# Kernel optimization log

Hardware: AMD Instinct MI355X
Metric: run time of the kernel (lower is better)

Reference implementation:

```python
import jax, jax.numpy as jnp
import numpy as np

T, IN, E, H, L = 8192, 40, 256, 512, 2


def setup_inputs() -> dict:
    key = jax.random.key(0)
    ks = jax.random.split(key, 12)
    s = lambda k, shape, scale: jax.random.normal(k, shape, dtype=jnp.float32) * scale
    return {
        "in_states": jax.random.normal(ks[0], (T, IN), dtype=jnp.float32),
        "W_in": s(ks[1], (E, IN), 0.1),
        "b_in": jnp.zeros((E,), jnp.float32),          # nn.Linear bias init to 0
        "W_ih0": s(ks[2], (4 * H, E), 0.04),
        "W_hh0": s(ks[3], (4 * H, H), 0.04),
        "b_ih0": s(ks[4], (4 * H,), 0.04),
        "b_hh0": s(ks[5], (4 * H,), 0.04),
        "W_ih1": s(ks[6], (4 * H, H), 0.04),
        "W_hh1": s(ks[7], (4 * H, H), 0.04),
        "b_ih1": s(ks[8], (4 * H,), 0.04),
        "b_hh1": s(ks[9], (4 * H,), 0.04),
        "W_out": s(ks[10], (1, H), 0.04),
        "b_out": jnp.zeros((1,), jnp.float32),         # nn.Linear bias init to 0
    }


def lstm_layer(x, W_ih, W_hh, b_ih, b_hh):
    """PyTorch-convention LSTM layer over a [T, in] sequence, batch=1.
    Gate order: i, f, g, o. Returns ([T, H] hidden seq, h_T, c_T)."""
    Hd = W_hh.shape[1]
    # Precompute the input contribution for all timesteps at once: [T, 4H]
    xg = x @ W_ih.T + (b_ih + b_hh)

    def cell(carry, xg_t):
        h, c = carry
        g = xg_t + h @ W_hh.T
        i, f, gg, o = jnp.split(g, 4)
        i = jax.nn.sigmoid(i)
        f = jax.nn.sigmoid(f)
        gg = jnp.tanh(gg)
        o = jax.nn.sigmoid(o)
        c = f * c + i * gg
        h = o * jnp.tanh(c)
        return (h, c), h

    h0 = jnp.zeros((Hd,), x.dtype)
    (hT, cT), hs = jax.lax.scan(cell, (h0, h0), xg)
    return hs, hT, cT


def reference(in_states, W_in, b_in, W_ih0, W_hh0, b_ih0, b_hh0,
              W_ih1, W_hh1, b_ih1, b_hh1, W_out, b_out):
    # Input projection for every timestep (the per-step nn.Linear, batched): [T, E]
    x = in_states @ W_in.T + b_in
    # Two stacked LSTM layers
    h1, hT0, cT0 = lstm_layer(x, W_ih0, W_hh0, b_ih0, b_hh0)
    h2, hT1, cT1 = lstm_layer(h1, W_ih1, W_hh1, b_ih1, b_hh1)
    # Output projection per timestep -> [T, 1, 1] like the torch `outputs` buffer
    outputs = (h2 @ W_out.T + b_out)[:, None, :]
    # Final hidden state tuple, shaped [num_layers, batch=1, H]
    h_final = jnp.stack([hT0, hT1])[:, None, :]
    c_final = jnp.stack([cT0, cT1])[:, None, :]
    return outputs, (h_final, c_final)
```

## Files before the change

kernel.cpp:

```cpp
#include <hip/hip_runtime.h>

#define T_LEN 8192
#define NIN   40
#define E_DIM 256
#define HID   512
#define G4H   2048

__device__ __forceinline__ float4 ld4_sc(const float* p) {
  float4 v;
  asm volatile("global_load_dwordx4 %0, %1, off sc0 sc1" : "=v"(v) : "v"(p));
  return v;
}
__device__ __forceinline__ unsigned ld_flag(const unsigned* p) {
  unsigned v;
  asm volatile("global_load_dword %0, %1, off sc0 sc1\n\ts_waitcnt vmcnt(0)"
               : "=v"(v) : "v"(p) : "memory");
  return v;
}
__device__ __forceinline__ void st_sc(float* p, float v) {
  asm volatile("global_store_dword %0, %1, off sc0 sc1" :: "v"(p), "v"(v) : "memory");
}
__device__ __forceinline__ void st_flag(unsigned* p, unsigned v) {
  asm volatile("global_store_dword %0, %1, off sc0 sc1" :: "v"(p), "v"(v) : "memory");
}
#define VM_FENCE() do { asm volatile("s_waitcnt vmcnt(0)" ::: "memory"); \
                        __builtin_amdgcn_sched_barrier(0); } while (0)

__device__ __forceinline__ float sigm(float x) {
  x = fminf(20.f, fmaxf(-20.f, x));
  float e = __builtin_amdgcn_exp2f(-1.442695040888963f * x);
  return __builtin_amdgcn_rcpf(1.f + e);
}
__device__ __forceinline__ float tanh_f(float x) {
  x = fminf(10.f, fmaxf(-10.f, x));
  float e = __builtin_amdgcn_exp2f(-2.885390081777927f * x);
  return (1.f - e) * __builtin_amdgcn_rcpf(1.f + e);
}
__device__ __forceinline__ float sel4(int k, float a0, float a1, float a2, float a3) {
  float r = a0;
  r = (k == 1) ? a1 : r;
  r = (k == 2) ? a2 : r;
  r = (k == 3) ? a3 : r;
  return r;
}

__global__ __launch_bounds__(64) void prep_kernel(
    const float* __restrict__ W_in, const float* __restrict__ b_in,
    const float* __restrict__ W_ih0, const float* __restrict__ b_ih0,
    const float* __restrict__ b_hh0,
    float* __restrict__ W_comb, float* __restrict__ bias_comb)
{
  const int r = blockIdx.x;
  const int lane = threadIdx.x;
  float bp = 0.f;
  for (int e = lane; e < E_DIM; e += 64) bp += W_ih0[(size_t)r * E_DIM + e] * b_in[e];
  float acc = 0.f;
  if (lane < NIN) {
    for (int e = 0; e < E_DIM; ++e)
      acc += W_ih0[(size_t)r * E_DIM + e] * W_in[(size_t)e * NIN + lane];
  }
#pragma unroll
  for (int m = 1; m < 64; m <<= 1) bp += __shfl_xor(bp, m, 64);
  if (lane < NIN) W_comb[(size_t)r * NIN + lane] = acc;
  if (lane == 0) bias_comb[r] = bp + b_ih0[r] + b_hh0[r];
}

__global__ __launch_bounds__(1024, 4) void scan_kernel(
    const float* __restrict__ in_states,
    const float* __restrict__ W_hh0,
    const float* __restrict__ W_ih1,
    const float* __restrict__ W_hh1,
    const float* __restrict__ b_ih1,
    const float* __restrict__ b_hh1,
    const float* __restrict__ W_comb,
    const float* __restrict__ bias_comb,
    float* __restrict__ h1buf, float* __restrict__ h2buf,
    unsigned* __restrict__ flags0, unsigned* __restrict__ flags1,
    float* __restrict__ d_out)
{
  const int tid  = threadIdx.x;
  const int wid  = tid >> 6;
  const int lane = tid & 63;
  const int bid  = blockIdx.x;

  __shared__ float lds_wcomb[128 * (NIN + 1)];
  __shared__ float lds_in[NIN];
  __shared__ float lds_indot[128];

  if (bid < 16) {
    const int u0 = bid * 32;
    const int uA = u0 + wid * 2;
    const int G  = (lane & 2) | ((lane >> 2) & 1);
    const int ulocal4 = (wid * 2 + (lane & 1)) * 4;

    for (int i = tid; i < 128 * NIN; i += 1024) {
      int lr = i / NIN, k = i - lr * NIN;
      int R = (lr & 3) * HID + u0 + (lr >> 2);
      lds_wcomb[lr * (NIN + 1) + k] = W_comb[(size_t)R * NIN + k];
    }
    float w[8][8];
#pragma unroll
    for (int q = 0; q < 8; ++q) {
      int R = (q & 3) * HID + uA + (q >> 2);
      const float4* p = (const float4*)(W_hh0 + (size_t)R * HID + lane * 8);
      float4 a = p[0], b = p[1];
      w[q][0]=a.x; w[q][1]=a.y; w[q][2]=a.z; w[q][3]=a.w;
      w[q][4]=b.x; w[q][5]=b.y; w[q][6]=b.z; w[q][7]=b.w;
    }
    float my_bias = 0.f;
    if (tid >= 128 && tid < 256) {
      int r = tid - 128;
      my_bias = bias_comb[(size_t)((r & 3) * HID + u0 + (r >> 2))];
    }
    float inreg = 0.f;
    if (tid >= 64 && tid < 64 + NIN) inreg = in_states[NIN + (tid - 64)];
    if (tid < NIN) lds_in[tid] = in_states[tid];
    __syncthreads();
    if (tid >= 128 && tid < 256) {
      int r = tid - 128;
      float s = my_bias;
#pragma unroll
      for (int k = 0; k < NIN; ++k) s += lds_wcomb[r * (NIN + 1) + k] * lds_in[k];
      lds_indot[r] = s;
    }

    float c_reg = 0.f;
    for (int t = 0; t < T_LEN; ++t) {
      if (wid == 0 && t > 0 && lane < 16) {
        const unsigned* fp = flags0 + (size_t)(t - 1) * 16 + lane;
        while (ld_flag(fp) == 0u) {}
      }
      __syncthreads();
      if (tid >= 64 && tid < 64 + NIN) {
        lds_in[tid - 64] = inreg;
        int t2 = (t + 2 < T_LEN) ? (t + 2) : (T_LEN - 1);
        inreg = in_states[(size_t)t2 * NIN + (tid - 64)];
      }
      float hv[8];
      if (t > 0) {
        const float* hp = h1buf + (size_t)(t - 1) * HID + lane * 8;
        float4 A = ld4_sc(hp);
        float4 B = ld4_sc(hp + 4);
        VM_FENCE();
        hv[0]=A.x; hv[1]=A.y; hv[2]=A.z; hv[3]=A.w;
        hv[4]=B.x; hv[5]=B.y; hv[6]=B.z; hv[7]=B.w;
      } else {
#pragma unroll
        for (int j = 0; j < 8; ++j) hv[j] = 0.f;
      }
      float acc[8] = {0,0,0,0,0,0,0,0};
#pragma unroll
      for (int cc = 0; cc < 8; ++cc) {
#pragma unroll
        for (int q = 0; q < 8; ++q) acc[q] = fmaf(w[q][cc], hv[cc], acc[q]);
      }
      float a4[4];
#pragma unroll
      for (int g = 0; g < 4; ++g) {
        float send = (lane & 1) ? acc[g] : acc[g + 4];
        float recv = __shfl_xor(send, 1, 64);
        a4[g] = ((lane & 1) ? acc[g + 4] : acc[g]) + recv;
      }
      float b2[2];
#pragma unroll
      for (int j = 0; j < 2; ++j) {
        float send = (lane & 2) ? a4[j] : a4[j + 2];
        float recv = __shfl_xor(send, 2, 64);
        b2[j] = ((lane & 2) ? a4[j + 2] : a4[j]) + recv;
      }
      float c1;
      {
        float send = (lane & 4) ? b2[0] : b2[1];
        float recv = __shfl_xor(send, 4, 64);
        c1 = ((lane & 4) ? b2[1] : b2[0]) + recv;
      }
      c1 += __shfl_xor(c1, 8, 64);
      c1 += __shfl_xor(c1, 16, 64);
      c1 += __shfl_xor(c1, 32, 64);
      float pre = c1 + lds_indot[ulocal4 + G];
      float s2 = __shfl_xor(pre, 2, 64);
      float s4 = __shfl_xor(pre, 4, 64);
      float s6 = __shfl_xor(pre, 6, 64);
      float prei = sel4(G,     pre, s4, s2, s6);
      float pref = sel4(G ^ 1, pre, s4, s2, s6);
      float preg = sel4(G ^ 2, pre, s4, s2, s6);
      float preo = sel4(G ^ 3, pre, s4, s2, s6);
      float gi = sigm(prei), gf = sigm(pref), gg = tanh_f(preg), go = sigm(preo);
      c_reg = gf * c_reg + gi * gg;
      float hnew = go * tanh_f(c_reg);
      if (lane < 2) {
        st_sc(h1buf + (size_t)t * HID + uA + lane, hnew);
        if (t == T_LEN - 1) {
          d_out[T_LEN + uA + lane] = hnew;
          d_out[T_LEN + 2 * HID + uA + lane] = c_reg;
        }
      }
      VM_FENCE();
      __syncthreads();
      if (tid == 0) st_flag(flags0 + (size_t)t * 16 + bid, 1u);
      if (tid >= 128 && tid < 256 && t + 1 < T_LEN) {
        int r = tid - 128;
        float s = my_bias;
#pragma unroll
        for (int k = 0; k < NIN; ++k) s += lds_wcomb[r * (NIN + 1) + k] * lds_in[k];
        lds_indot[r] = s;
      }
    }
  } else {
    const int wg = bid - 16;
    const int u0 = wg * 16;
    const int u  = u0 + wid;
    const int G  = ((lane & 1) << 1) | ((lane >> 1) & 1);
    float w[4][16];
    {
      const float* Wsrc = (lane < 32) ? W_ih1 : W_hh1;
      int colbase = (lane & 31) * 16;
#pragma unroll
      for (int g = 0; g < 4; ++g) {
        int R = g * HID + u;
        const float4* p = (const float4*)(Wsrc + (size_t)R * HID + colbase);
        float4 x0 = p[0], x1 = p[1], x2 = p[2], x3 = p[3];
        w[g][0]=x0.x;  w[g][1]=x0.y;  w[g][2]=x0.z;  w[g][3]=x0.w;
        w[g][4]=x1.x;  w[g][5]=x1.y;  w[g][6]=x1.z;  w[g][7]=x1.w;
        w[g][8]=x2.x;  w[g][9]=x2.y;  w[g][10]=x2.z; w[g][11]=x2.w;
        w[g][12]=x3.x; w[g][13]=x3.y; w[g][14]=x3.z; w[g][15]=x3.w;
      }
    }
    const float bias_lane = b_ih1[G * HID + u] + b_hh1[G * HID + u];
    float c_reg = 0.f;
    for (int t = 0; t < T_LEN; ++t) {
      if (wid == 0) {
        const unsigned* fp = nullptr;
        if (lane < 16) fp = flags0 + (size_t)t * 16 + lane;
        else if (lane < 48 && t > 0) fp = flags1 + (size_t)(t - 1) * 32 + (lane - 16);
        if (fp) { while (ld_flag(fp) == 0u) {} }
      }
      __syncthreads();
      float hv[16];
      {
        int col = (lane & 31) * 16;
        int tp = (t > 0) ? (t - 1) : 0;
        const float* hp = (lane < 32) ? (h1buf + (size_t)t * HID + col)
                                      : (h2buf + (size_t)tp * HID + col);
        bool hvalid = (lane < 32) || (t > 0);
        float4 A = ld4_sc(hp);
        float4 B = ld4_sc(hp + 4);
        float4 C = ld4_sc(hp + 8);
        float4 D = ld4_sc(hp + 12);
        VM_FENCE();
        float tmp[16];
        tmp[0]=A.x; tmp[1]=A.y; tmp[2]=A.z; tmp[3]=A.w;
        tmp[4]=B.x; tmp[5]=B.y; tmp[6]=B.z; tmp[7]=B.w;
        tmp[8]=C.x; tmp[9]=C.y; tmp[10]=C.z; tmp[11]=C.w;
        tmp[12]=D.x; tmp[13]=D.y; tmp[14]=D.z; tmp[15]=D.w;
#pragma unroll
        for (int j = 0; j < 16; ++j) hv[j] = hvalid ? tmp[j] : 0.f;
      }
      float acc[4] = {0,0,0,0};
#pragma unroll
      for (int cc = 0; cc < 16; ++cc) {
#pragma unroll
        for (int g = 0; g < 4; ++g) acc[g] = fmaf(w[g][cc], hv[cc], acc[g]);
      }
      float b2[2];
#pragma unroll
      for (int j = 0; j < 2; ++j) {
        float send = (lane & 1) ? acc[j] : acc[j + 2];
        float recv = __shfl_xor(send, 1, 64);
        b2[j] = ((lane & 1) ? acc[j + 2] : acc[j]) + recv;
      }
      float c1;
      {
        float send = (lane & 2) ? b2[0] : b2[1];
        float recv = __shfl_xor(send, 2, 64);
        c1 = ((lane & 2) ? b2[1] : b2[0]) + recv;
      }
      c1 += __shfl_xor(c1, 4, 64);
      c1 += __shfl_xor(c1, 8, 64);
      c1 += __shfl_xor(c1, 16, 64);
      c1 += __shfl_xor(c1, 32, 64);
      float pre = c1 + bias_lane;
      float s1 = __shfl_xor(pre, 1, 64);
      float s2 = __shfl_xor(pre, 2, 64);
      float s3 = __shfl_xor(pre, 3, 64);
      float prei = sel4(G,     pre, s2, s1, s3);
      float pref = sel4(G ^ 1, pre, s2, s1, s3);
      float preg = sel4(G ^ 2, pre, s2, s1, s3);
      float preo = sel4(G ^ 3, pre, s2, s1, s3);
      float gi = sigm(prei), gf = sigm(pref), gg = tanh_f(preg), go = sigm(preo);
      c_reg = gf * c_reg + gi * gg;
      float hnew = go * tanh_f(c_reg);
      if (lane == 0) {
        st_sc(h2buf + (size_t)t * HID + u, hnew);
        if (t == T_LEN - 1) {
          d_out[T_LEN + HID + u] = hnew;
          d_out[T_LEN + 3 * HID + u] = c_reg;
        }
      }
      VM_FENCE();
      __syncthreads();
      if (tid == 0) st_flag(flags1 + (size_t)t * 32 + wg, 1u);
    }
  }
}

__global__ __launch_bounds__(256) void out_kernel(
    const float* __restrict__ h2buf, const float* __restrict__ W_out,
    const float* __restrict__ b_out, float* __restrict__ d_out)
{
  int t = blockIdx.x * 4 + (threadIdx.x >> 6);
  int lane = threadIdx.x & 63;
  const float4* hp = (const float4*)(h2buf + (size_t)t * HID + lane * 8);
  const float4* wp = (const float4*)(W_out + lane * 8);
  float4 a = hp[0], b = hp[1], wa = wp[0], wb = wp[1];
  float s = a.x*wa.x + a.y*wa.y + a.z*wa.z + a.w*wa.w
          + b.x*wb.x + b.y*wb.y + b.z*wb.z + b.w*wb.w;
#pragma unroll
  for (int m = 1; m < 64; m <<= 1) s += __shfl_xor(s, m, 64);
  if (lane == 0) d_out[t] = s + b_out[0];
}

extern "C" void kernel_launch(void* const* d_in, const int* in_sizes, int n_in,
                              void* d_out, int out_size, void* d_ws, size_t ws_size,
                              hipStream_t stream) {
  const float* in_states = (const float*)d_in[0];
  const float* W_in  = (const float*)d_in[1];
  const float* b_in  = (const float*)d_in[2];
  const float* W_ih0 = (const float*)d_in[3];
  const float* W_hh0 = (const float*)d_in[4];
  const float* b_ih0 = (const float*)d_in[5];
  const float* b_hh0 = (const float*)d_in[6];
  const float* W_ih1 = (const float*)d_in[7];
  const float* W_hh1 = (const float*)d_in[8];
  const float* b_ih1 = (const float*)d_in[9];
  const float* b_hh1 = (const float*)d_in[10];
  const float* W_out = (const float*)d_in[11];
  const float* b_out = (const float*)d_in[12];

  float* ws = (float*)d_ws;
  size_t o = 0;
  float* W_comb = ws + o;    o += (size_t)G4H * NIN;
  float* bias_comb = ws + o; o += G4H;
  float* h1buf = ws + o;     o += (size_t)T_LEN * HID;
  float* h2buf = ws + o;     o += (size_t)T_LEN * HID;
  unsigned* flags0 = (unsigned*)(ws + o); o += (size_t)T_LEN * 16;
  unsigned* flags1 = (unsigned*)(ws + o); o += (size_t)T_LEN * 32;

  hipMemsetAsync(flags0, 0, (size_t)T_LEN * 48 * sizeof(unsigned), stream);

  prep_kernel<<<G4H, 64, 0, stream>>>(W_in, b_in, W_ih0, b_ih0, b_hh0,
                                      W_comb, bias_comb);
  scan_kernel<<<48, 1024, 0, stream>>>(in_states, W_hh0, W_ih1, W_hh1,
                                       b_ih1, b_hh1, W_comb, bias_comb,
                                       h1buf, h2buf, flags0, flags1,
                                       (float*)d_out);
  out_kernel<<<2048, 256, 0, stream>>>(h2buf, W_out, b_out, (float*)d_out);
}
```

Before: 25.22 ms.

## Replace flag barriers with sequence-tagged data polling across single-wave blocks

Restructures the persistent LSTM scan so each single-wave block owns two hidden units, with 512 blocks instead of 48 large blocks. Each hidden value is stored next to a sequence tag, so consumers poll the data itself rather than separate flag arrays behind __syncthreads, removing a round trip and the block-level barriers. The input projection is folded into the per-step FMA, layer 2 uses an 8-slot ring buffer, and the output projection becomes per-step atomics, removing the separate output kernel. The risks are heavier polling traffic from 512 spinning waves, possible deadlock if not all blocks are co-resident, and atomic ordering making the output sum order nondeterministic.

```diff
diff --git a/kernel.cpp b/kernel.cpp
--- a/kernel.cpp
+++ b/kernel.cpp
@@ -5,23 +5,17 @@
 #define E_DIM 256
 #define HID   512
 #define G4H   2048
+#define RD    8
 
 __device__ __forceinline__ float4 ld4_sc(const float* p) {
   float4 v;
   asm volatile("global_load_dwordx4 %0, %1, off sc0 sc1" : "=v"(v) : "v"(p));
   return v;
 }
-__device__ __forceinline__ unsigned ld_flag(const unsigned* p) {
-  unsigned v;
-  asm volatile("global_load_dword %0, %1, off sc0 sc1\n\ts_waitcnt vmcnt(0)"
-               : "=v"(v) : "v"(p) : "memory");
-  return v;
-}
-__device__ __forceinline__ void st_sc(float* p, float v) {
-  asm volatile("global_store_dword %0, %1, off sc0 sc1" :: "v"(p), "v"(v) : "memory");
-}
-__device__ __forceinline__ void st_flag(unsigned* p, unsigned v) {
-  asm volatile("global_store_dword %0, %1, off sc0 sc1" :: "v"(p), "v"(v) : "memory");
+__device__ __forceinline__ void st2_sc(float* p, float h, unsigned seq) {
+  union { float2 f; uint2 u; } pv;
+  pv.u.x = __float_as_uint(h); pv.u.y = seq;
+  asm volatile("global_store_dwordx2 %0, %1, off sc0 sc1" :: "v"(p), "v"(pv.f) : "memory");
 }
 #define VM_FENCE() do { asm volatile("s_waitcnt vmcnt(0)" ::: "memory"); \
                         __builtin_amdgcn_sched_barrier(0); } while (0)
@@ -65,7 +59,7 @@
   if (lane == 0) bias_comb[r] = bp + b_ih0[r] + b_hh0[r];
 }
 
-__global__ __launch_bounds__(1024, 4) void scan_kernel(
+__global__ __launch_bounds__(64, 1) void scan_kernel(
     const float* __restrict__ in_states,
     const float* __restrict__ W_hh0,
     const float* __restrict__ W_ih1,
@@ -74,30 +68,18 @@
     const float* __restrict__ b_hh1,
     const float* __restrict__ W_comb,
     const float* __restrict__ bias_comb,
-    float* __restrict__ h1buf, float* __restrict__ h2buf,
-    unsigned* __restrict__ flags0, unsigned* __restrict__ flags1,
+    const float* __restrict__ W_out,
+    const float* __restrict__ b_out,
+    float* __restrict__ h1pair,
+    float* __restrict__ h2ring,
     float* __restrict__ d_out)
 {
-  const int tid  = threadIdx.x;
-  const int wid  = tid >> 6;
-  const int lane = tid & 63;
+  const int lane = threadIdx.x;
   const int bid  = blockIdx.x;
-
-  __shared__ float lds_wcomb[128 * (NIN + 1)];
-  __shared__ float lds_in[NIN];
-  __shared__ float lds_indot[128];
-
-  if (bid < 16) {
-    const int u0 = bid * 32;
-    const int uA = u0 + wid * 2;
-    const int G  = (lane & 2) | ((lane >> 2) & 1);
-    const int ulocal4 = (wid * 2 + (lane & 1)) * 4;
-
-    for (int i = tid; i < 128 * NIN; i += 1024) {
-      int lr = i / NIN, k = i - lr * NIN;
-      int R = (lr & 3) * HID + u0 + (lr >> 2);
-      lds_wcomb[lr * (NIN + 1) + k] = W_comb[(size_t)R * NIN + k];
-    }
+  const int G    = (lane & 2) | ((lane >> 2) & 1);
+
+  if (bid < 256) {
+    const int uA = bid * 2;
     float w[8][8];
 #pragma unroll
     for (int q = 0; q < 8; ++q) {
@@ -107,48 +89,42 @@
       w[q][0]=a.x; w[q][1]=a.y; w[q][2]=a.z; w[q][3]=a.w;
       w[q][4]=b.x; w[q][5]=b.y; w[q][6]=b.z; w[q][7]=b.w;
     }
-    float my_bias = 0.f;
-    if (tid >= 128 && tid < 256) {
-      int r = tid - 128;
-      my_bias = bias_comb[(size_t)((r & 3) * HID + u0 + (r >> 2))];
-    }
-    float inreg = 0.f;
-    if (tid >= 64 && tid < 64 + NIN) inreg = in_states[NIN + (tid - 64)];
-    if (tid < NIN) lds_in[tid] = in_states[tid];
-    __syncthreads();
-    if (tid >= 128 && tid < 256) {
-      int r = tid - 128;
-      float s = my_bias;
-#pragma unroll
-      for (int k = 0; k < NIN; ++k) s += lds_wcomb[r * (NIN + 1) + k] * lds_in[k];
-      lds_indot[r] = s;
-    }
-
+    float w2[8];
+#pragma unroll
+    for (int q = 0; q < 8; ++q) {
+      int R = (q & 3) * HID + uA + (q >> 2);
+      w2[q] = (lane < NIN) ? W_comb[(size_t)R * NIN + lane] : 0.f;
+    }
+    const float bias_lane = bias_comb[G * HID + uA + (lane & 1)];
+    float in_cur = (lane < NIN) ? in_states[lane] : 0.f;
     float c_reg = 0.f;
+
     for (int t = 0; t < T_LEN; ++t) {
-      if (wid == 0 && t > 0 && lane < 16) {
-        const unsigned* fp = flags0 + (size_t)(t - 1) * 16 + lane;
-        while (ld_flag(fp) == 0u) {}
-      }
-      __syncthreads();
-      if (tid >= 64 && tid < 64 + NIN) {
-        lds_in[tid - 64] = inreg;
-        int t2 = (t + 2 < T_LEN) ? (t + 2) : (T_LEN - 1);
-        inreg = in_states[(size_t)t2 * NIN + (tid - 64)];
-      }
+      float in_nxt = (lane < NIN && t + 1 < T_LEN)
+                   ? in_states[(size_t)(t + 1) * NIN + lane] : 0.f;
       float hv[8];
       if (t > 0) {
-        const float* hp = h1buf + (size_t)(t - 1) * HID + lane * 8;
-        float4 A = ld4_sc(hp);
-        float4 B = ld4_sc(hp + 4);
-        VM_FENCE();
-        hv[0]=A.x; hv[1]=A.y; hv[2]=A.z; hv[3]=A.w;
-        hv[4]=B.x; hv[5]=B.y; hv[6]=B.z; hv[7]=B.w;
+        const float* hp = h1pair + ((size_t)(t - 1) << 10) + lane * 16;
+        const unsigned e = (unsigned)t;
+        float4 A, B, C, D; int ok;
+        do {
+          A = ld4_sc(hp); B = ld4_sc(hp + 4); C = ld4_sc(hp + 8); D = ld4_sc(hp + 12);
+          VM_FENCE();
+          unsigned bad = (__float_as_uint(A.y) ^ e) | (__float_as_uint(A.w) ^ e)
+                       | (__float_as_uint(B.y) ^ e) | (__float_as_uint(B.w) ^ e)
+                       | (__float_as_uint(C.y) ^ e) | (__float_as_uint(C.w) ^ e)
+                       | (__float_as_uint(D.y) ^ e) | (__float_as_uint(D.w) ^ e);
+          ok = (bad == 0u);
+        } while (!__all(ok));
+        hv[0]=A.x; hv[1]=A.z; hv[2]=B.x; hv[3]=B.z;
+        hv[4]=C.x; hv[5]=C.z; hv[6]=D.x; hv[7]=D.z;
       } else {
 #pragma unroll
         for (int j = 0; j < 8; ++j) hv[j] = 0.f;
       }
-      float acc[8] = {0,0,0,0,0,0,0,0};
+      float acc[8];
+#pragma unroll
+      for (int q = 0; q < 8; ++q) acc[q] = w2[q] * in_cur;
 #pragma unroll
       for (int cc = 0; cc < 8; ++cc) {
 #pragma unroll
@@ -177,7 +153,7 @@
       c1 += __shfl_xor(c1, 8, 64);
       c1 += __shfl_xor(c1, 16, 64);
       c1 += __shfl_xor(c1, 32, 64);
-      float pre = c1 + lds_indot[ulocal4 + G];
+      float pre = c1 + bias_lane;
       float s2 = __shfl_xor(pre, 2, 64);
       float s4 = __shfl_xor(pre, 4, 64);
       float s6 = __shfl_xor(pre, 6, 64);
@@ -189,135 +165,121 @@
       c_reg = gf * c_reg + gi * gg;
       float hnew = go * tanh_f(c_reg);
       if (lane < 2) {
-        st_sc(h1buf + (size_t)t * HID + uA + lane, hnew);
+        st2_sc(h1pair + ((size_t)t << 10) + (uA + lane) * 2, hnew, (unsigned)(t + 1));
         if (t == T_LEN - 1) {
           d_out[T_LEN + uA + lane] = hnew;
           d_out[T_LEN + 2 * HID + uA + lane] = c_reg;
         }
       }
-      VM_FENCE();
-      __syncthreads();
-      if (tid == 0) st_flag(flags0 + (size_t)t * 16 + bid, 1u);
-      if (tid >= 128 && tid < 256 && t + 1 < T_LEN) {
-        int r = tid - 128;
-        float s = my_bias;
-#pragma unroll
-        for (int k = 0; k < NIN; ++k) s += lds_wcomb[r * (NIN + 1) + k] * lds_in[k];
-        lds_indot[r] = s;
-      }
+      in_cur = in_nxt;
     }
   } else {
-    const int wg = bid - 16;
-    const int u0 = wg * 16;
-    const int u  = u0 + wid;
-    const int G  = ((lane & 1) << 1) | ((lane >> 1) & 1);
-    float w[4][16];
-    {
-      const float* Wsrc = (lane < 32) ? W_ih1 : W_hh1;
-      int colbase = (lane & 31) * 16;
+    const int uB = (bid - 256) * 2;
+    const float* Wsrc = (lane < 32) ? W_ih1 : W_hh1;
+    const int c0 = (lane & 31) * 16;
+    float w[8][16];
+#pragma unroll
+    for (int q = 0; q < 8; ++q) {
+      int R = (q & 3) * HID + uB + (q >> 2);
+      const float4* p = (const float4*)(Wsrc + (size_t)R * HID + c0);
+      float4 x0 = p[0], x1 = p[1], x2 = p[2], x3 = p[3];
+      w[q][0]=x0.x;  w[q][1]=x0.y;  w[q][2]=x0.z;  w[q][3]=x0.w;
+      w[q][4]=x1.x;  w[q][5]=x1.y;  w[q][6]=x1.z;  w[q][7]=x1.w;
+      w[q][8]=x2.x;  w[q][9]=x2.y;  w[q][10]=x2.z; w[q][11]=x2.w;
+      w[q][12]=x3.x; w[q][13]=x3.y; w[q][14]=x3.z; w[q][15]=x3.w;
+    }
+    const int brow = G * HID + uB + (lane & 1);
+    const float bias_lane = b_ih1[brow] + b_hh1[brow];
+    const float wout_lane = W_out[uB + (lane & 1)];
+    const float b_out0 = b_out[0];
+    float c_reg = 0.f;
+
+    for (int t = 0; t < T_LEN; ++t) {
+      const bool is_h1 = (lane < 32);
+      const bool hvalid = is_h1 || (t > 0);
+      const int rslot = (t > 0) ? ((t - 1) % RD) : 0;
+      const float* hp = is_h1
+          ? (h1pair + ((size_t)t << 10) + lane * 32)
+          : (h2ring + (size_t)rslot * 1024 + (lane - 32) * 32);
+      const unsigned e = is_h1 ? (unsigned)(t + 1) : (unsigned)t;
+      float4 P0, P1, P2, P3, P4, P5, P6, P7; int ok;
+      do {
+        P0 = ld4_sc(hp);      P1 = ld4_sc(hp + 4);
+        P2 = ld4_sc(hp + 8);  P3 = ld4_sc(hp + 12);
+        P4 = ld4_sc(hp + 16); P5 = ld4_sc(hp + 20);
+        P6 = ld4_sc(hp + 24); P7 = ld4_sc(hp + 28);
+        VM_FENCE();
+        unsigned bad = (__float_as_uint(P0.y) ^ e) | (__float_as_uint(P0.w) ^ e)
+                     | (__float_as_uint(P1.y) ^ e) | (__float_as_uint(P1.w) ^ e)
+                     | (__float_as_uint(P2.y) ^ e) | (__float_as_uint(P2.w) ^ e)
+                     | (__float_as_uint(P3.y) ^ e) | (__float_as_uint(P3.w) ^ e)
+                     | (__float_as_uint(P4.y) ^ e) | (__float_as_uint(P4.w) ^ e)
+                     | (__float_as_uint(P5.y) ^ e) | (__float_as_uint(P5.w) ^ e)
+                     | (__float_as_uint(P6.y) ^ e) | (__float_as_uint(P6.w) ^ e)
+                     | (__float_as_uint(P7.y) ^ e) | (__float_as_uint(P7.w) ^ e);
+        ok = (bad == 0u) || !hvalid;
+      } while (!__all(ok));
+      float hv[16];
+      hv[0]=P0.x;  hv[1]=P0.z;  hv[2]=P1.x;  hv[3]=P1.z;
+      hv[4]=P2.x;  hv[5]=P2.z;  hv[6]=P3.x;  hv[7]=P3.z;
+      hv[8]=P4.x;  hv[9]=P4.z;  hv[10]=P5.x; hv[11]=P5.z;
+      hv[12]=P6.x; hv[13]=P6.z; hv[14]=P7.x; hv[15]=P7.z;
+      if (!hvalid) {
+#pragma unroll
+        for (int j = 0; j < 16; ++j) hv[j] = 0.f;
+      }
+      float acc[8] = {0,0,0,0,0,0,0,0};
+#pragma unroll
+      for (int cc = 0; cc < 16; ++cc) {
+#pragma unroll
+        for (int q = 0; q < 8; ++q) acc[q] = fmaf(w[q][cc], hv[cc], acc[q]);
+      }
+      float a4[4];
 #pragma unroll
       for (int g = 0; g < 4; ++g) {
-        int R = g * HID + u;
-        const float4* p = (const float4*)(Wsrc + (size_t)R * HID + colbase);
-        float4 x0 = p[0], x1 = p[1], x2 = p[2], x3 = p[3];
-        w[g][0]=x0.x;  w[g][1]=x0.y;  w[g][2]=x0.z;  w[g][3]=x0.w;
-        w[g][4]=x1.x;  w[g][5]=x1.y;  w[g][6]=x1.z;  w[g][7]=x1.w;
-        w[g][8]=x2.x;  w[g][9]=x2.y;  w[g][10]=x2.z; w[g][11]=x2.w;
-        w[g][12]=x3.x; w[g][13]=x3.y; w[g][14]=x3.z; w[g][15]=x3.w;
-      }
-    }
-    const float bias_lane = b_ih1[G * HID + u] + b_hh1[G * HID + u];
-    float c_reg = 0.f;
-    for (int t = 0; t < T_LEN; ++t) {
-      if (wid == 0) {
-        const unsigned* fp = nullptr;
-        if (lane < 16) fp = flags0 + (size_t)t * 16 + lane;
-        else if (lane < 48 && t > 0) fp = flags1 + (size_t)(t - 1) * 32 + (lane - 16);
-        if (fp) { while (ld_flag(fp) == 0u) {} }
-      }
-      __syncthreads();
-      float hv[16];
-      {
-        int col = (lane & 31) * 16;
-        int tp = (t > 0) ? (t - 1) : 0;
-        const float* hp = (lane < 32) ? (h1buf + (size_t)t * HID + col)
-                                      : (h2buf + (size_t)tp * HID + col);
-        bool hvalid = (lane < 32) || (t > 0);
-        float4 A = ld4_sc(hp);
-        float4 B = ld4_sc(hp + 4);
-        float4 C = ld4_sc(hp + 8);
-        float4 D = ld4_sc(hp + 12);
-        VM_FENCE();
-        float tmp[16];
-        tmp[0]=A.x; tmp[1]=A.y; tmp[2]=A.z; tmp[3]=A.w;
-        tmp[4]=B.x; tmp[5]=B.y; tmp[6]=B.z; tmp[7]=B.w;
-        tmp[8]=C.x; tmp[9]=C.y; tmp[10]=C.z; tmp[11]=C.w;
-        tmp[12]=D.x; tmp[13]=D.y; tmp[14]=D.z; tmp[15]=D.w;
-#pragma unroll
-        for (int j = 0; j < 16; ++j) hv[j] = hvalid ? tmp[j] : 0.f;
-      }
-      float acc[4] = {0,0,0,0};
-#pragma unroll
-      for (int cc = 0; cc < 16; ++cc) {
-#pragma unroll
-        for (int g = 0; g < 4; ++g) acc[g] = fmaf(w[g][cc], hv[cc], acc[g]);
-      }
-      float b2[2];
+        float send = (lane & 1) ? acc[g] : acc[g + 4];
+        float recv = __shfl_xor(send, 1, 64);
+        a4[g] = ((lane & 1) ? acc[g + 4] : acc[g]) + recv;
+      }
+      float b2v[2];
 #pragma unroll
       for (int j = 0; j < 2; ++j) {
-        float send = (lane & 1) ? acc[j] : acc[j + 2];
-        float recv = __shfl_xor(send, 1, 64);
-        b2[j] = ((lane & 1) ? acc[j + 2] : acc[j]) + recv;
+        float send = (lane & 2) ? a4[j] : a4[j + 2];
+        float recv = __shfl_xor(send, 2, 64);
+        b2v[j] = ((lane & 2) ? a4[j + 2] : a4[j]) + recv;
       }
       float c1;
       {
-        float send = (lane & 2) ? b2[0] : b2[1];
-        float recv = __shfl_xor(send, 2, 64);
-        c1 = ((lane & 2) ? b2[1] : b2[0]) + recv;
-      }
-      c1 += __shfl_xor(c1, 4, 64);
+        float send = (lane & 4) ? b2v[0] : b2v[1];
+        float recv = __shfl_xor(send, 4, 64);
+        c1 = ((lane & 4) ? b2v[1] : b2v[0]) + recv;
+      }
       c1 += __shfl_xor(c1, 8, 64);
       c1 += __shfl_xor(c1, 16, 64);
       c1 += __shfl_xor(c1, 32, 64);
       float pre = c1 + bias_lane;
-      float s1 = __shfl_xor(pre, 1, 64);
       float s2 = __shfl_xor(pre, 2, 64);
-      float s3 = __shfl_xor(pre, 3, 64);
-      float prei = sel4(G,     pre, s2, s1, s3);
-      float pref = sel4(G ^ 1, pre, s2, s1, s3);
-      float preg = sel4(G ^ 2, pre, s2, s1, s3);
-      float preo = sel4(G ^ 3, pre, s2, s1, s3);
+      float s4 = __shfl_xor(pre, 4, 64);
+      float s6 = __shfl_xor(pre, 6, 64);
+      float prei = sel4(G,     pre, s4, s2, s6);
+      float pref = sel4(G ^ 1, pre, s4, s2, s6);
+      float preg = sel4(G ^ 2, pre, s4, s2, s6);
+      float preo = sel4(G ^ 3, pre, s4, s2, s6);
       float gi = sigm(prei), gf = sigm(pref), gg = tanh_f(preg), go = sigm(preo);
       c_reg = gf * c_reg + gi * gg;
       float hnew = go * tanh_f(c_reg);
-      if (lane == 0) {
-        st_sc(h2buf + (size_t)t * HID + u, hnew);
+      float v = hnew * wout_lane;
+      v += __shfl_xor(v, 1, 64);
+      if (lane == 0) atomicAdd(d_out + t, (uB == 0) ? (v + b_out0) : v);
+      if (lane < 2) {
+        st2_sc(h2ring + (size_t)(t % RD) * 1024 + (uB + lane) * 2, hnew, (unsigned)(t + 1));
         if (t == T_LEN - 1) {
-          d_out[T_LEN + HID + u] = hnew;
-          d_out[T_LEN + 3 * HID + u] = c_reg;
+          d_out[T_LEN + HID + uB + lane] = hnew;
+          d_out[T_LEN + 3 * HID + uB + lane] = c_reg;
         }
       }
-      VM_FENCE();
-      __syncthreads();
-      if (tid == 0) st_flag(flags1 + (size_t)t * 32 + wg, 1u);
     }
   }
-}
-
-__global__ __launch_bounds__(256) void out_kernel(
-    const float* __restrict__ h2buf, const float* __restrict__ W_out,
-    const float* __restrict__ b_out, float* __restrict__ d_out)
-{
-  int t = blockIdx.x * 4 + (threadIdx.x >> 6);
-  int lane = threadIdx.x & 63;
-  const float4* hp = (const float4*)(h2buf + (size_t)t * HID + lane * 8);
-  const float4* wp = (const float4*)(W_out + lane * 8);
-  float4 a = hp[0], b = hp[1], wa = wp[0], wb = wp[1];
-  float s = a.x*wa.x + a.y*wa.y + a.z*wa.z + a.w*wa.w
-          + b.x*wb.x + b.y*wb.y + b.z*wb.z + b.w*wb.w;
-#pragma unroll
-  for (int m = 1; m < 64; m <<= 1) s += __shfl_xor(s, m, 64);
-  if (lane == 0) d_out[t] = s + b_out[0];
 }
 
 extern "C" void kernel_launch(void* const* d_in, const int* in_sizes, int n_in,
@@ -341,18 +303,15 @@
   size_t o = 0;
   float* W_comb = ws + o;    o += (size_t)G4H * NIN;
   float* bias_comb = ws + o; o += G4H;
-  float* h1buf = ws + o;     o += (size_t)T_LEN * HID;
-  float* h2buf = ws + o;     o += (size_t)T_LEN * HID;
-  unsigned* flags0 = (unsigned*)(ws + o); o += (size_t)T_LEN * 16;
-  unsigned* flags1 = (unsigned*)(ws + o); o += (size_t)T_LEN * 32;
-
-  hipMemsetAsync(flags0, 0, (size_t)T_LEN * 48 * sizeof(unsigned), stream);
+  float* h1pair = ws + o;    o += (size_t)T_LEN * HID * 2;
+  float* h2ring = ws + o;    o += (size_t)RD * HID * 2;
+
+  hipMemsetAsync(d_out, 0, (size_t)T_LEN * sizeof(float), stream);
 
   prep_kernel<<<G4H, 64, 0, stream>>>(W_in, b_in, W_ih0, b_ih0, b_hh0,
                                       W_comb, bias_comb);
-  scan_kernel<<<48, 1024, 0, stream>>>(in_states, W_hh0, W_ih1, W_hh1,
-                                       b_ih1, b_hh1, W_comb, bias_comb,
-                                       h1buf, h2buf, flags0, flags1,
-                                       (float*)d_out);
-  out_kernel<<<2048, 256, 0, stream>>>(h2buf, W_out, b_out, (float*)d_out);
-}
+  scan_kernel<<<512, 64, 0, stream>>>(in_states, W_hh0, W_ih1, W_hh1,
+                                      b_ih1, b_hh1, W_comb, bias_comb,
+                                      W_out, b_out,
+                                      h1pair, h2ring, (float*)d_out);
+}
```

Result: slower. 48.34 ms (+91.6%).
